# Kernel tuning notes

Measured on AMD Instinct MI355X. Metric: run time of the kernel, lower is better.

Reference implementation:

```python
import math
import jax, jax.numpy as jnp
import numpy as np

B, S, D, H = 2, 2048, 2048, 16
HD = D // H
SCALE = 1.0 / math.sqrt(HD)


def setup_inputs() -> dict:
    key = jax.random.key(0)
    kx, kq, kk, kv, ko = jax.random.split(key, 5)
    w_std = 1.0 / math.sqrt(D)
    return {
        "x": jax.random.normal(kx, (B, S, D), jnp.float32),
        "Wq": jax.random.normal(kq, (D, D), jnp.float32) * w_std,
        "Wk": jax.random.normal(kk, (D, D), jnp.float32) * w_std,
        "Wv": jax.random.normal(kv, (D, D), jnp.float32) * w_std,
        "Wo": jax.random.normal(ko, (D, D), jnp.float32) * w_std,
        "attention_mask": jnp.ones((B, S), jnp.int32),
        "sliding_window": 512,
        "sink_tokens": 4,
    }


def reference(x, Wq, Wk, Wv, Wo, attention_mask, sliding_window, sink_tokens):
    b, s, d = x.shape
    # nn.Linear(bias=False): y = x @ W^T
    q = (x @ Wq.T).reshape(b, s, H, HD).transpose(0, 2, 1, 3)  # [b,h,s,hd]
    k = (x @ Wk.T).reshape(b, s, H, HD).transpose(0, 2, 1, 3)
    v = (x @ Wv.T).reshape(b, s, H, HD).transpose(0, 2, 1, 3)

    scores = jnp.einsum("bhqd,bhkd->bhqk", q, k) * SCALE  # [b,h,s,s]

    i = jnp.arange(s)[:, None]
    j = jnp.arange(s)[None, :]
    causal = j <= i
    window = (j >= i - sliding_window + 1) & (j <= i)
    # sink mask in the source fills [0:i+1] for every row (rows < sink_tokens
    # and rows >= sink_tokens alike), i.e. it is identical to the causal mask.
    sink = causal
    allowed = causal & window & sink  # [s,s]
    pad = (attention_mask != 0)[:, None, None, :]  # [b,1,1,s]
    scores = jnp.where(allowed[None, None] & pad, scores, -jnp.inf)

    attn = jax.nn.softmax(scores, axis=-1)
    out = jnp.einsum("bhqk,bhkd->bhqd", attn, v)  # [b,h,s,hd]
    out = out.transpose(0, 2, 1, 3).reshape(b, s, d)
    return out @ Wo.T
```

## Files before the change

kernel.cpp:

```cpp
#include <hip/hip_runtime.h>
#include <stdint.h>


typedef __attribute__((ext_vector_type(8))) short short8;
typedef __attribute__((ext_vector_type(4))) float f32x4;

#define DEV static __device__ __forceinline__

DEV unsigned short f2bf(float f) {
  unsigned u = __builtin_bit_cast(unsigned, f);
  u += 0x7fffu + ((u >> 16) & 1u);
  return (unsigned short)(u >> 16);
}

DEV void async16(const void* g, void* l) {
  __builtin_amdgcn_global_load_lds(
      (const __attribute__((address_space(1))) unsigned int*)g,
      (__attribute__((address_space(3))) unsigned int*)l, 16, 0, 0);
}

__global__ __launch_bounds__(256) void cast_all(
    const float* __restrict__ x, const float* __restrict__ Wq,
    const float* __restrict__ Wk, const float* __restrict__ Wv,
    const float* __restrict__ Wo, unsigned short* __restrict__ xb,
    unsigned short* __restrict__ wqkv, unsigned short* __restrict__ wob) {
  const int bid = blockIdx.x;
  const float* src;
  unsigned short* dst;
  int i;
  if (bid < 4096) {
    src = x; dst = xb; i = bid * 256 + threadIdx.x;
  } else if (bid < 6144) {
    src = Wq; dst = wqkv; i = (bid - 4096) * 256 + threadIdx.x;
  } else if (bid < 8192) {
    src = Wk; dst = wqkv + 4194304; i = (bid - 6144) * 256 + threadIdx.x;
  } else if (bid < 10240) {
    src = Wv; dst = wqkv + 8388608; i = (bid - 8192) * 256 + threadIdx.x;
  } else {
    src = Wo; dst = wob; i = (bid - 10240) * 256 + threadIdx.x;
  }
  const float4* s4 = (const float4*)src;
  float4 a = s4[2 * (size_t)i], b = s4[2 * (size_t)i + 1];
  short8 o;
  o[0] = (short)f2bf(a.x); o[1] = (short)f2bf(a.y);
  o[2] = (short)f2bf(a.z); o[3] = (short)f2bf(a.w);
  o[4] = (short)f2bf(b.x); o[5] = (short)f2bf(b.y);
  o[6] = (short)f2bf(b.z); o[7] = (short)f2bf(b.w);
  *(short8*)(dst + 8 * (size_t)i) = o;
}

constexpr int GK = 2048, GN = 2048;

#define MFMA_BF16 __builtin_amdgcn_mfma_f32_16x16x32_bf16

#define STAGE_A(buf, h, kt)                                                  \
  {                                                                          \
    const unsigned short* g_ = Ag + (size_t)((h) * 128) * GK + (kt) * 64;    \
    char* d_ = (char*)As[buf] + (h) * 16384 + loff;                          \
    async16(g_, d_);                                                         \
    async16(g_ + (size_t)64 * GK, d_ + 8192);                                \
  }
#define STAGE_B(buf, h, kt)                                                  \
  {                                                                          \
    const unsigned short* g_ = Bg + (size_t)((h) * 128) * GK + (kt) * 64;    \
    char* d_ = (char*)Bs[buf] + (h) * 16384 + loff;                          \
    async16(g_, d_);                                                         \
    async16(g_ + (size_t)64 * GK, d_ + 8192);                                \
  }

#define READ_A(buf, mq_)                                                     \
  _Pragma("unroll") for (int mi = 0; mi < 4; ++mi)                           \
      _Pragma("unroll") for (int kc = 0; kc < 2; ++kc) afr[mi][kc] =         \
      *(const short8*)(As[buf] + (mq_)*4096 + aoff[mi][kc]);
#define READ_B01(buf)                                                        \
  _Pragma("unroll") for (int ni = 0; ni < 2; ++ni)                           \
      _Pragma("unroll") for (int kc = 0; kc < 2; ++kc) bfr[ni][kc] =         \
      *(const short8*)(Bs[buf] + boff[ni][kc]);
#define READ_B23(buf)                                                        \
  _Pragma("unroll") for (int ni = 2; ni < 4; ++ni)                           \
      _Pragma("unroll") for (int kc = 0; kc < 2; ++kc) bfr[ni][kc] =         \
      *(const short8*)(Bs[buf] + boff[ni][kc]);

#define PH_MFMA(mq_, nq_)                                                    \
  __builtin_amdgcn_s_setprio(1);                                             \
  _Pragma("unroll") for (int mi = 0; mi < 4; ++mi)                           \
      _Pragma("unroll") for (int ni = 0; ni < 2; ++ni) {                     \
    acc[(mq_)*4 + mi][(nq_)*2 + ni] =                                        \
        MFMA_BF16(afr[mi][0], bfr[(nq_)*2 + ni][0],                          \
                  acc[(mq_)*4 + mi][(nq_)*2 + ni], 0, 0, 0);                 \
    acc[(mq_)*4 + mi][(nq_)*2 + ni] =                                        \
        MFMA_BF16(afr[mi][1], bfr[(nq_)*2 + ni][1],                          \
                  acc[(mq_)*4 + mi][(nq_)*2 + ni], 0, 0, 0);                 \
  }                                                                          \
  __builtin_amdgcn_s_setprio(0);

#define BAR __builtin_amdgcn_s_barrier();
#define LGKM0 __asm__ __volatile__("s_waitcnt lgkmcnt(0)" ::: "memory");
#define VM(n) __asm__ __volatile__("s_waitcnt vmcnt(" #n ")" ::: "memory");

template <bool STORE_BF16>
__global__ __launch_bounds__(512, 2) void gemm256(
    const unsigned short* __restrict__ A, const unsigned short* __restrict__ B,
    void* __restrict__ Cout, size_t obuf_stride) {
  __shared__ short As[2][16384];
  __shared__ short Bs[2][16384];

  const int t = threadIdx.x;
  const int lane = t & 63;
  const int quad = lane >> 4, l15 = lane & 15, l7 = l15 & 7;
  const int w = t >> 6, wm = w >> 2, wn = w & 3;

  const int nwg = (int)gridDim.x;
  const int cpx = nwg >> 3;
  const int swz = ((int)blockIdx.x & 7) * cpx + ((int)blockIdx.x >> 3);
  const int bx = swz & 15, by = swz >> 4;
  const int row0 = bx * 256, col0g = by * 256;
  const int nb = col0g >> 11, col0 = col0g & 2047;

  const int rsub = t >> 3;
  const int cg8 = ((t & 7) ^ (rsub & 7)) << 3;
  const unsigned short* Ag = A + (size_t)(row0 + rsub) * GK + cg8;
  const unsigned short* Bg = B + (size_t)(col0g + rsub) * GK + cg8;
  const int loff = rsub * 128 + (t & 7) * 16;

  int aoff[4][2], boff[4][2];
#pragma unroll
  for (int mi = 0; mi < 4; ++mi)
#pragma unroll
    for (int kc = 0; kc < 2; ++kc)
      aoff[mi][kc] =
          (wm * 128 + mi * 16 + l15) * 64 + (((kc * 4 + quad) ^ l7) << 3);
#pragma unroll
  for (int ni = 0; ni < 4; ++ni)
#pragma unroll
    for (int kc = 0; kc < 2; ++kc)
      boff[ni][kc] =
          (wn * 64 + ni * 16 + l15) * 64 + (((kc * 4 + quad) ^ l7) << 3);

  f32x4 acc[8][4] = {};
  short8 afr[4][2], bfr[4][2];

  STAGE_A(0, 0, 0) STAGE_A(0, 1, 0)
  STAGE_B(0, 0, 0) STAGE_B(0, 1, 0)
  STAGE_B(1, 0, 1) STAGE_B(1, 1, 1)
  VM(4)
  BAR

  for (int i = 0; i < 15; ++i) {
    const int t1 = 2 * i + 1;
    READ_A(0, 0) READ_B01(0)
    STAGE_A(1, 0, t1)
    BAR LGKM0
    PH_MFMA(0, 0)
    BAR
    READ_B23(0)
    STAGE_A(1, 1, t1)
    BAR LGKM0
    PH_MFMA(0, 1)
    BAR
    READ_A(0, 1)
    STAGE_B(0, 0, t1 + 1)
    BAR LGKM0
    PH_MFMA(1, 0)
    BAR
    STAGE_B(0, 1, t1 + 1)
    VM(4)
    BAR
    PH_MFMA(1, 1)
    BAR
    READ_A(1, 0) READ_B01(1)
    STAGE_A(0, 0, t1 + 1)
    BAR LGKM0
    PH_MFMA(0, 0)
    BAR
    READ_B23(1)
    STAGE_A(0, 1, t1 + 1)
    BAR LGKM0
    PH_MFMA(0, 1)
    BAR
    READ_A(1, 1)
    STAGE_B(1, 0, t1 + 2)
    BAR LGKM0
    PH_MFMA(1, 0)
    BAR
    STAGE_B(1, 1, t1 + 2)
    VM(4)
    BAR
    PH_MFMA(1, 1)
    BAR
  }

  {
    READ_A(0, 0) READ_B01(0)
    STAGE_A(1, 0, 31)
    BAR LGKM0
    PH_MFMA(0, 0)
    BAR
    READ_B23(0)
    STAGE_A(1, 1, 31)
    BAR LGKM0
    PH_MFMA(0, 1)
    BAR
    READ_A(0, 1)
    BAR LGKM0
    PH_MFMA(1, 0)
    BAR
    VM(0)
    BAR
    PH_MFMA(1, 1)
    BAR
    READ_A(1, 0) READ_B01(1)
    BAR LGKM0
    PH_MFMA(0, 0)
    BAR
    READ_B23(1)
    BAR LGKM0
    PH_MFMA(0, 1)
    BAR
    READ_A(1, 1)
    BAR LGKM0
    PH_MFMA(1, 0)
    BAR
    PH_MFMA(1, 1)
  }

#pragma unroll
  for (int MI = 0; MI < 8; ++MI)
#pragma unroll
    for (int ni = 0; ni < 4; ++ni)
#pragma unroll
      for (int r = 0; r < 4; ++r) {
        int row = row0 + wm * 128 + MI * 16 + quad * 4 + r;
        int col = col0 + wn * 64 + ni * 16 + l15;
        if (STORE_BF16)
          ((unsigned short*)Cout)[nb * obuf_stride + (size_t)row * GN + col] =
              f2bf(acc[MI][ni][r]);
        else
          ((float*)Cout)[nb * obuf_stride + (size_t)row * GN + col] =
              acc[MI][ni][r];
      }
}

__global__ __launch_bounds__(256) void transpose_v(
    const unsigned short* __restrict__ vb, unsigned short* __restrict__ vtb) {
  __shared__ unsigned short tile[64][72];
  const int s0 = blockIdx.x * 64, d0 = blockIdx.y * 64, b = blockIdx.z;
  const int tid = threadIdx.x;
  const int c8 = tid & 7;
#pragma unroll
  for (int i = 0; i < 2; ++i) {
    int row = i * 32 + (tid >> 3);
    uint4 v = *(const uint4*)(vb + (size_t)(b * 2048 + s0 + row) * 2048 + d0 + c8 * 8);
    *(uint4*)&tile[row][c8 * 8] = v;
  }
  __syncthreads();
#pragma unroll
  for (int i = 0; i < 2; ++i) {
    int dr = i * 32 + (tid >> 3);
    short8 sv;
#pragma unroll
    for (int j = 0; j < 8; ++j) sv[j] = (short)tile[c8 * 8 + j][dr];
    int d = d0 + dr;
    int h = d >> 7, hd = d & 127;
    *(short8*)(vtb + ((size_t)(b * 16 + h) * 128 + hd) * 2048 + s0 + c8 * 8) = sv;
  }
}

__global__ __launch_bounds__(256, 3) void attn_mfma(
    const unsigned short* __restrict__ Qm, const unsigned short* __restrict__ Km,
    const unsigned short* __restrict__ Vt, unsigned short* __restrict__ Om,
    const int* __restrict__ amask, const int* __restrict__ winp) {
  constexpr int S = 2048, D = 2048, HD = 128;
  const float SCALE = 0.08838834764831845f;

  __shared__ short Ks[64 * 128];
  __shared__ short Vts[128 * 64];
  __shared__ short Ps[4][16 * 64];

  const int t = threadIdx.x, w = t >> 6, lane = t & 63;
  const int quad = lane >> 4, l15 = lane & 15;
  const int l7 = l15 & 7;
  const int f = blockIdx.x;
  const int qt = f >> 5, g = f & 31;
  const int h = g & 15, b = g >> 4;
  const int qi0 = qt * 64;
  const int win = winp[0];

  short8 qf[4];
  {
    const unsigned short* qp =
        Qm + (size_t)(b * S + qi0 + w * 16 + l15) * D + h * HD + quad * 8;
#pragma unroll
    for (int kc = 0; kc < 4; ++kc) qf[kc] = *(const short8*)(qp + kc * 32);
  }

  f32x4 o[8] = {};
  float m_r[4], l_r[4];
#pragma unroll
  for (int r = 0; r < 4; ++r) { m_r[r] = -1e30f; l_r[r] = 0.f; }

  int lowj = qi0 - win + 1;
  if (lowj < 0) lowj = 0;
  const int jt0 = lowj >> 6;

  const int krow = lane >> 4, kpos = lane & 15;
  const int vrow = lane >> 3, vpos = lane & 7;

  for (int jt = jt0; jt <= qt; ++jt) {
    const int j0 = jt * 64;
    __syncthreads();
#pragma unroll
    for (int ii = 0; ii < 4; ++ii) {
      int row = ii * 16 + w * 4 + krow;
      int c = kpos ^ (row & 7);
      async16(Km + (size_t)(b * S + j0 + row) * D + h * HD + c * 8,
              (char*)Ks + (ii * 16 + w * 4) * 256);
    }
#pragma unroll
    for (int ii = 0; ii < 4; ++ii) {
      int row = ii * 32 + w * 8 + vrow;
      int c = vpos ^ (row & 7);
      async16(Vt + ((size_t)(b * 16 + h) * 128 + row) * S + j0 + c * 8,
              (char*)Vts + (ii * 32 + w * 8) * 128);
    }
    __syncthreads();

    f32x4 sS[4];
#pragma unroll
    for (int ni = 0; ni < 4; ++ni) {
      f32x4 acc = {0.f, 0.f, 0.f, 0.f};
#pragma unroll
      for (int kc = 0; kc < 4; ++kc) {
        int pos = (kc * 4 + quad) ^ l7;
        short8 bk = *(const short8*)&Ks[(ni * 16 + l15) * 128 + pos * 8];
        acc = __builtin_amdgcn_mfma_f32_16x16x32_bf16(qf[kc], bk, acc, 0, 0, 0);
      }
      sS[ni] = acc;
    }

    float sv[4][4];
    int amv[4];
#pragma unroll
    for (int ni = 0; ni < 4; ++ni) amv[ni] = amask[b * S + j0 + ni * 16 + l15];
#pragma unroll
    for (int ni = 0; ni < 4; ++ni)
#pragma unroll
      for (int r = 0; r < 4; ++r) {
        int gi = qi0 + w * 16 + quad * 4 + r;
        int gj = j0 + ni * 16 + l15;
        bool ok = (gj <= gi) && (gj >= gi - win + 1) && (amv[ni] != 0);
        sv[ni][r] = ok ? sS[ni][r] * SCALE : -1e30f;
      }
    float alpha[4], mnew[4];
#pragma unroll
    for (int r = 0; r < 4; ++r) {
      float mx = fmaxf(fmaxf(sv[0][r], sv[1][r]), fmaxf(sv[2][r], sv[3][r]));
      mx = fmaxf(mx, __shfl_xor(mx, 1));
      mx = fmaxf(mx, __shfl_xor(mx, 2));
      mx = fmaxf(mx, __shfl_xor(mx, 4));
      mx = fmaxf(mx, __shfl_xor(mx, 8));
      float mn = fmaxf(m_r[r], mx);
      alpha[r] = __expf(m_r[r] - mn);
      m_r[r] = mn;
      mnew[r] = mn;
    }
    float rs[4] = {0.f, 0.f, 0.f, 0.f};
#pragma unroll
    for (int ni = 0; ni < 4; ++ni)
#pragma unroll
      for (int r = 0; r < 4; ++r) {
        float p = (sv[ni][r] > -1e29f) ? __expf(sv[ni][r] - mnew[r]) : 0.f;
        sv[ni][r] = p;
        rs[r] += p;
      }
#pragma unroll
    for (int r = 0; r < 4; ++r) {
      float s = rs[r];
      s += __shfl_xor(s, 1);
      s += __shfl_xor(s, 2);
      s += __shfl_xor(s, 4);
      s += __shfl_xor(s, 8);
      l_r[r] = l_r[r] * alpha[r] + s;
    }
#pragma unroll
    for (int ni = 0; ni < 4; ++ni)
#pragma unroll
      for (int r = 0; r < 4; ++r) {
        int row = quad * 4 + r;
        int col = ni * 16 + l15;
        int pos = (col >> 3) ^ (row & 7);
        Ps[w][row * 64 + pos * 8 + (col & 7)] = (short)f2bf(sv[ni][r]);
      }
#pragma unroll
    for (int ni2 = 0; ni2 < 8; ++ni2)
#pragma unroll
      for (int r = 0; r < 4; ++r) o[ni2][r] *= alpha[r];

    __asm__ __volatile__("s_waitcnt lgkmcnt(0)" ::: "memory");

    short8 aP[2];
#pragma unroll
    for (int kc2 = 0; kc2 < 2; ++kc2) {
      int pos = (kc2 * 4 + quad) ^ l7;
      aP[kc2] = *(const short8*)&Ps[w][l15 * 64 + pos * 8];
    }
#pragma unroll
    for (int ni2 = 0; ni2 < 8; ++ni2) {
#pragma unroll
      for (int kc2 = 0; kc2 < 2; ++kc2) {
        int pos = (kc2 * 4 + quad) ^ l7;
        short8 bv = *(const short8*)&Vts[(ni2 * 16 + l15) * 64 + pos * 8];
        o[ni2] = __builtin_amdgcn_mfma_f32_16x16x32_bf16(aP[kc2], bv, o[ni2], 0, 0, 0);
      }
    }
  }

  float inv[4];
#pragma unroll
  for (int r = 0; r < 4; ++r) inv[r] = 1.f / l_r[r];
#pragma unroll
  for (int ni2 = 0; ni2 < 8; ++ni2)
#pragma unroll
    for (int r = 0; r < 4; ++r) {
      int row = qi0 + w * 16 + quad * 4 + r;
      Om[(size_t)(b * S + row) * D + h * HD + ni2 * 16 + l15] =
          f2bf(o[ni2][r] * inv[r]);
    }
}

extern "C" void kernel_launch(void* const* d_in, const int* in_sizes, int n_in,
                              void* d_out, int out_size, void* d_ws,
                              size_t ws_size, hipStream_t stream) {
  (void)in_sizes; (void)n_in; (void)out_size; (void)ws_size;
  const float* x  = (const float*)d_in[0];
  const float* Wq = (const float*)d_in[1];
  const float* Wk = (const float*)d_in[2];
  const float* Wv = (const float*)d_in[3];
  const float* Wo = (const float*)d_in[4];
  const int* am   = (const int*)d_in[5];
  const int* win  = (const int*)d_in[6];

  char* ws = (char*)d_ws;
  unsigned short* xb   = (unsigned short*)(ws + 0);
  unsigned short* vtb  = (unsigned short*)(ws + 0);
  unsigned short* wqkv = (unsigned short*)(ws + 16777216);
  unsigned short* wob  = (unsigned short*)(ws + 41943040);
  unsigned short* qb   = (unsigned short*)(ws + 50331648);
  unsigned short* kb   = (unsigned short*)(ws + 67108864);
  unsigned short* vb   = (unsigned short*)(ws + 83886080);
  unsigned short* ab   = (unsigned short*)(ws + 100663296);

  cast_all<<<dim3(12288), dim3(256), 0, stream>>>(x, Wq, Wk, Wv, Wo, xb, wqkv, wob);

  gemm256<true><<<dim3(384), dim3(512), 0, stream>>>(xb, wqkv, qb, 8388608);

  transpose_v<<<dim3(32, 32, 2), dim3(256), 0, stream>>>(vb, vtb);

  attn_mfma<<<dim3(1024), dim3(256), 0, stream>>>(qb, kb, vtb, ab, am, win);

  gemm256<false><<<dim3(128), dim3(512), 0, stream>>>(ab, wob, d_out, 0);
}
```

Before: 378.8 us.

## Software-pipeline LDS fragment reads with MFMAs in gemm256 and halve barriers

Restructures the GEMM main loop so each phase issues LDS reads for the next k-chunk fragments (double-buffered register sets afA/afB, b0/b1) while running 16 MFMAs on the current ones. This removes the second barrier per phase and the exposed wait between LDS reads and MFMAs. Fragment offsets shrink to per-kc bases, which saves registers. The risk is more complex ordering correctness around barriers and buffer reuse, plus higher register pressure from two fragment sets.

After: 370.0 us. 2.3% less time.

```diff
diff --git a/kernel.cpp b/kernel.cpp
--- a/kernel.cpp
+++ b/kernel.cpp
@@ -68,33 +68,23 @@
     async16(g_ + (size_t)64 * GK, d_ + 8192);                                \
   }
 
-#define READ_A(buf, mq_)                                                     \
+#define READ_AF(dst, buf, mq, kc)                                            \
+  _Pragma("unroll") for (int mi = 0; mi < 4; ++mi) dst[mi] =                 \
+      *(const short8*)(As[buf] + aoffk[kc] + (mq)*4096 + mi * 1024);
+#define READ_BF(dst, buf, kc)                                                \
+  _Pragma("unroll") for (int ni = 0; ni < 4; ++ni) dst[ni] =                 \
+      *(const short8*)(Bs[buf] + boffk[kc] + ni * 1024);
+
+#define MFMA16(mq, A_, B_)                                                   \
   _Pragma("unroll") for (int mi = 0; mi < 4; ++mi)                           \
-      _Pragma("unroll") for (int kc = 0; kc < 2; ++kc) afr[mi][kc] =         \
-      *(const short8*)(As[buf] + (mq_)*4096 + aoff[mi][kc]);
-#define READ_B01(buf)                                                        \
-  _Pragma("unroll") for (int ni = 0; ni < 2; ++ni)                           \
-      _Pragma("unroll") for (int kc = 0; kc < 2; ++kc) bfr[ni][kc] =         \
-      *(const short8*)(Bs[buf] + boff[ni][kc]);
-#define READ_B23(buf)                                                        \
-  _Pragma("unroll") for (int ni = 2; ni < 4; ++ni)                           \
-      _Pragma("unroll") for (int kc = 0; kc < 2; ++kc) bfr[ni][kc] =         \
-      *(const short8*)(Bs[buf] + boff[ni][kc]);
-
-#define PH_MFMA(mq_, nq_)                                                    \
-  __builtin_amdgcn_s_setprio(1);                                             \
-  _Pragma("unroll") for (int mi = 0; mi < 4; ++mi)                           \
-      _Pragma("unroll") for (int ni = 0; ni < 2; ++ni) {                     \
-    acc[(mq_)*4 + mi][(nq_)*2 + ni] =                                        \
-        MFMA_BF16(afr[mi][0], bfr[(nq_)*2 + ni][0],                          \
-                  acc[(mq_)*4 + mi][(nq_)*2 + ni], 0, 0, 0);                 \
-    acc[(mq_)*4 + mi][(nq_)*2 + ni] =                                        \
-        MFMA_BF16(afr[mi][1], bfr[(nq_)*2 + ni][1],                          \
-                  acc[(mq_)*4 + mi][(nq_)*2 + ni], 0, 0, 0);                 \
-  }                                                                          \
-  __builtin_amdgcn_s_setprio(0);
-
-#define BAR __builtin_amdgcn_s_barrier();
+      _Pragma("unroll") for (int ni = 0; ni < 4; ++ni)                       \
+      acc[(mq)*4 + mi][ni] =                                                 \
+      MFMA_BF16(A_[mi], B_[ni], acc[(mq)*4 + mi][ni], 0, 0, 0);
+
+#define MEMF __asm__ __volatile__("" ::: "memory");
+#define BARR { MEMF __builtin_amdgcn_s_barrier(); MEMF }
+#define SP1 __builtin_amdgcn_s_setprio(1);
+#define SP0 __builtin_amdgcn_s_setprio(0);
 #define LGKM0 __asm__ __volatile__("s_waitcnt lgkmcnt(0)" ::: "memory");
 #define VM(n) __asm__ __volatile__("s_waitcnt vmcnt(" #n ")" ::: "memory");
 
@@ -123,105 +113,76 @@
   const unsigned short* Bg = B + (size_t)(col0g + rsub) * GK + cg8;
   const int loff = rsub * 128 + (t & 7) * 16;
 
-  int aoff[4][2], boff[4][2];
-#pragma unroll
-  for (int mi = 0; mi < 4; ++mi)
-#pragma unroll
-    for (int kc = 0; kc < 2; ++kc)
-      aoff[mi][kc] =
-          (wm * 128 + mi * 16 + l15) * 64 + (((kc * 4 + quad) ^ l7) << 3);
-#pragma unroll
-  for (int ni = 0; ni < 4; ++ni)
-#pragma unroll
-    for (int kc = 0; kc < 2; ++kc)
-      boff[ni][kc] =
-          (wn * 64 + ni * 16 + l15) * 64 + (((kc * 4 + quad) ^ l7) << 3);
+  int aoffk[2], boffk[2];
+#pragma unroll
+  for (int kc = 0; kc < 2; ++kc) {
+    int swzc = (((kc * 4 + quad) ^ l7) << 3);
+    aoffk[kc] = wm * 8192 + l15 * 64 + swzc;
+    boffk[kc] = wn * 4096 + l15 * 64 + swzc;
+  }
 
   f32x4 acc[8][4] = {};
-  short8 afr[4][2], bfr[4][2];
+  short8 afA[4], afB[4], b0[4], b1[4];
 
   STAGE_A(0, 0, 0) STAGE_A(0, 1, 0)
   STAGE_B(0, 0, 0) STAGE_B(0, 1, 0)
   STAGE_B(1, 0, 1) STAGE_B(1, 1, 1)
   VM(4)
-  BAR
-
+  BARR
+  READ_AF(afA, 0, 0, 0) READ_BF(b0, 0, 0)
+  LGKM0
+
+#pragma unroll 1
   for (int i = 0; i < 15; ++i) {
     const int t1 = 2 * i + 1;
-    READ_A(0, 0) READ_B01(0)
     STAGE_A(1, 0, t1)
-    BAR LGKM0
-    PH_MFMA(0, 0)
-    BAR
-    READ_B23(0)
+    BARR
+    SP1 READ_AF(afB, 0, 0, 1) READ_BF(b1, 0, 1) MFMA16(0, afA, b0) SP0 LGKM0
     STAGE_A(1, 1, t1)
-    BAR LGKM0
-    PH_MFMA(0, 1)
-    BAR
-    READ_A(0, 1)
+    BARR
+    SP1 READ_AF(afA, 0, 1, 0) MFMA16(0, afB, b1) SP0 LGKM0
     STAGE_B(0, 0, t1 + 1)
-    BAR LGKM0
-    PH_MFMA(1, 0)
-    BAR
+    BARR
+    SP1 READ_AF(afB, 0, 1, 1) MFMA16(1, afA, b0) SP0 LGKM0
     STAGE_B(0, 1, t1 + 1)
     VM(4)
-    BAR
-    PH_MFMA(1, 1)
-    BAR
-    READ_A(1, 0) READ_B01(1)
+    BARR
+    SP1 READ_AF(afA, 1, 0, 0) READ_BF(b0, 1, 0) MFMA16(1, afB, b1) SP0 LGKM0
     STAGE_A(0, 0, t1 + 1)
-    BAR LGKM0
-    PH_MFMA(0, 0)
-    BAR
-    READ_B23(1)
+    BARR
+    SP1 READ_AF(afB, 1, 0, 1) READ_BF(b1, 1, 1) MFMA16(0, afA, b0) SP0 LGKM0
     STAGE_A(0, 1, t1 + 1)
-    BAR LGKM0
-    PH_MFMA(0, 1)
-    BAR
-    READ_A(1, 1)
+    BARR
+    SP1 READ_AF(afA, 1, 1, 0) MFMA16(0, afB, b1) SP0 LGKM0
     STAGE_B(1, 0, t1 + 2)
-    BAR LGKM0
-    PH_MFMA(1, 0)
-    BAR
+    BARR
+    SP1 READ_AF(afB, 1, 1, 1) MFMA16(1, afA, b0) SP0 LGKM0
     STAGE_B(1, 1, t1 + 2)
     VM(4)
-    BAR
-    PH_MFMA(1, 1)
-    BAR
+    BARR
+    SP1 READ_AF(afA, 0, 0, 0) READ_BF(b0, 0, 0) MFMA16(1, afB, b1) SP0 LGKM0
   }
 
   {
-    READ_A(0, 0) READ_B01(0)
     STAGE_A(1, 0, 31)
-    BAR LGKM0
-    PH_MFMA(0, 0)
-    BAR
-    READ_B23(0)
+    BARR
+    SP1 READ_AF(afB, 0, 0, 1) READ_BF(b1, 0, 1) MFMA16(0, afA, b0) SP0 LGKM0
     STAGE_A(1, 1, 31)
-    BAR LGKM0
-    PH_MFMA(0, 1)
-    BAR
-    READ_A(0, 1)
-    BAR LGKM0
-    PH_MFMA(1, 0)
-    BAR
+    BARR
+    SP1 READ_AF(afA, 0, 1, 0) MFMA16(0, afB, b1) SP0 LGKM0
+    BARR
+    SP1 READ_AF(afB, 0, 1, 1) MFMA16(1, afA, b0) SP0 LGKM0
     VM(0)
-    BAR
-    PH_MFMA(1, 1)
-    BAR
-    READ_A(1, 0) READ_B01(1)
-    BAR LGKM0
-    PH_MFMA(0, 0)
-    BAR
-    READ_B23(1)
-    BAR LGKM0
-    PH_MFMA(0, 1)
-    BAR
-    READ_A(1, 1)
-    BAR LGKM0
-    PH_MFMA(1, 0)
-    BAR
-    PH_MFMA(1, 1)
+    BARR
+    SP1 READ_AF(afA, 1, 0, 0) READ_BF(b0, 1, 0) MFMA16(1, afB, b1) SP0 LGKM0
+    BARR
+    SP1 READ_AF(afB, 1, 0, 1) READ_BF(b1, 1, 1) MFMA16(0, afA, b0) SP0 LGKM0
+    BARR
+    SP1 READ_AF(afA, 1, 1, 0) MFMA16(0, afB, b1) SP0 LGKM0
+    BARR
+    SP1 READ_AF(afB, 1, 1, 1) MFMA16(1, afA, b0) SP0 LGKM0
+    BARR
+    SP1 MFMA16(1, afB, b1) SP0
   }
 
 #pragma unroll
```
